# Kernel tuning notes

Measured on AMD Instinct MI355X. Metric: run time of the kernel, lower is better.

Reference implementation:

```python
import jax, jax.numpy as jnp
import numpy as np

D = 512      # dim_model
F = 2048     # dim_feedforward
E = 8        # num_experts
K = 2        # num_experts_per_token
B, S = 2, 4096


def setup_inputs() -> dict:
    key = jax.random.key(0)
    ks = jax.random.split(key, 8)
    sd = 1.0 / np.sqrt(D)
    sf = 1.0 / np.sqrt(F)
    return {
        "x": jax.random.normal(ks[0], (B, S, D), dtype=jnp.float32),
        "router_w": jax.random.uniform(ks[1], (D, E), jnp.float32, -sd, sd),
        "router_b": jax.random.uniform(ks[2], (E,), jnp.float32, -sd, sd),
        "w1": jax.random.uniform(ks[3], (E, D, F), jnp.float32, -sd, sd),
        "b1": jax.random.uniform(ks[4], (E, F), jnp.float32, -sd, sd),
        "w2": jax.random.uniform(ks[5], (E, F, D), jnp.float32, -sf, sf),
        "b2": jax.random.uniform(ks[6], (E, D), jnp.float32, -sf, sf),
    }


def reference(x, router_w, router_b, w1, b1, w2, b2):
    orig_shape = x.shape
    flat = x.reshape(-1, orig_shape[-1])                     # [T, D]
    logits = flat @ router_w + router_b                      # [T, E]
    gates = jax.nn.softmax(logits, axis=-1)                  # [T, E]
    top_vals, top_idx = jax.lax.top_k(gates, K)              # [T, K]
    top_vals = top_vals / jnp.sum(top_vals, axis=-1, keepdims=True)
    # combine weight per (token, expert): zero for unselected experts,
    # so dense per-expert evaluation yields identical math to masked dispatch.
    onehot = jax.nn.one_hot(top_idx, E, dtype=flat.dtype)    # [T, K, E]
    comb = jnp.einsum('tk,tke->te', top_vals, onehot)        # [T, E]
    # expert FFNs over all tokens (dropout is identity in eval)
    hidden = jax.nn.relu(jnp.einsum('td,edf->etf', flat, w1) + b1[:, None, :])  # [E, T, F]
    eout = jnp.einsum('etf,efd->etd', hidden, w2) + b2[:, None, :]              # [E, T, D]
    out = jnp.einsum('te,etd->td', comb, eout)               # [T, D]
    return out.reshape(orig_shape)
```

## Files before the change

kernel.cpp:

```cpp
#include <hip/hip_runtime.h>
#include <cstdint>
#include <cstddef>

#define TD 512
#define TF 2048
#define NE 8
#define NT 8192
#define CAP 17408

using u16 = unsigned short;
using u32 = unsigned int;

typedef __attribute__((ext_vector_type(8))) __bf16 bf16x8;
typedef __attribute__((ext_vector_type(4))) float f32x4;

__device__ __forceinline__ u16 f2bf(float f) {
  u32 u = __float_as_uint(f);
  u32 r = (u + 0x7fffu + ((u >> 16) & 1u)) >> 16;
  return (u16)r;
}

__device__ __forceinline__ void load_lds16(const void* g, void* l) {
  __builtin_amdgcn_global_load_lds(
      (const __attribute__((address_space(1))) void*)g,
      (__attribute__((address_space(3))) void*)l, 16, 0, 0);
}

__global__ void zero_kernel(float* __restrict__ out) {
  int i = blockIdx.x * 256 + threadIdx.x;
  float4 z = make_float4(0.f, 0.f, 0.f, 0.f);
  *reinterpret_cast<float4*>(out + (size_t)i * 4) = z;
}

__global__ void transpose_cvt_kernel(const float* __restrict__ in, u16* __restrict__ out,
                                     int R, int C) {
  __shared__ u16 tile[32][33];
  int c0 = blockIdx.x * 32, r0 = blockIdx.y * 32;
  const float* ib = in + (size_t)blockIdx.z * R * C;
  u16* ob = out + (size_t)blockIdx.z * R * C;
  #pragma unroll
  for (int rr = 0; rr < 32; rr += 8) {
    int r = r0 + threadIdx.y + rr;
    int c = c0 + threadIdx.x;
    tile[threadIdx.y + rr][threadIdx.x] = f2bf(ib[(size_t)r * C + c]);
  }
  __syncthreads();
  #pragma unroll
  for (int rr = 0; rr < 32; rr += 8) {
    int oc = c0 + threadIdx.y + rr;
    int orr = r0 + threadIdx.x;
    ob[(size_t)oc * R + orr] = tile[threadIdx.x][threadIdx.y + rr];
  }
}

__global__ void router_kernel(const float* __restrict__ x, const float* __restrict__ rw,
                              const float* __restrict__ rb, int2* __restrict__ tokE,
                              float2* __restrict__ tokG, u16* __restrict__ xb) {
  int wv = threadIdx.x >> 6;
  int lane = threadIdx.x & 63;
  int t = blockIdx.x * 4 + wv;
  const float* xr = x + (size_t)t * TD;
  float4 a0 = *reinterpret_cast<const float4*>(xr + lane * 4);
  float4 a1 = *reinterpret_cast<const float4*>(xr + 256 + lane * 4);
  {
    u16 o[8];
    o[0] = f2bf(a0.x); o[1] = f2bf(a0.y); o[2] = f2bf(a0.z); o[3] = f2bf(a0.w);
    o[4] = f2bf(a1.x); o[5] = f2bf(a1.y); o[6] = f2bf(a1.z); o[7] = f2bf(a1.w);
    u16* xo = xb + (size_t)t * TD;
    *reinterpret_cast<uint2*>(xo + lane * 4) = *reinterpret_cast<uint2*>(o);
    *reinterpret_cast<uint2*>(xo + 256 + lane * 4) = *reinterpret_cast<uint2*>(o + 4);
  }
  float p[NE];
  #pragma unroll
  for (int e = 0; e < NE; e++) p[e] = 0.f;
  float av[8] = {a0.x, a0.y, a0.z, a0.w, a1.x, a1.y, a1.z, a1.w};
  #pragma unroll
  for (int j = 0; j < 8; j++) {
    int d = (j < 4) ? (lane * 4 + j) : (256 + lane * 4 + j - 4);
    const float* r = rw + (size_t)d * NE;
    #pragma unroll
    for (int e = 0; e < NE; e++) p[e] += av[j] * r[e];
  }
  #pragma unroll
  for (int off = 32; off >= 1; off >>= 1) {
    #pragma unroll
    for (int e = 0; e < NE; e++) p[e] += __shfl_xor(p[e], off);
  }
  if (lane == 0) {
    float l[NE];
    #pragma unroll
    for (int e = 0; e < NE; e++) l[e] = p[e] + rb[e];
    float m = l[0];
    #pragma unroll
    for (int e = 1; e < NE; e++) m = fmaxf(m, l[e]);
    float g[NE];
    #pragma unroll
    for (int e = 0; e < NE; e++) g[e] = __expf(l[e] - m);
    int i0 = 0;
    #pragma unroll
    for (int e = 1; e < NE; e++) if (g[e] > g[i0]) i0 = e;
    int i1 = -1;
    #pragma unroll
    for (int e = 0; e < NE; e++) {
      if (e == i0) continue;
      if (i1 < 0 || g[e] > g[i1]) i1 = e;
    }
    float inv = 1.f / (g[i0] + g[i1]);
    tokE[t] = make_int2(i0, i1);
    tokG[t] = make_float2(g[i0] * inv, g[i1] * inv);
  }
}

__global__ void count_offsets_kernel(const int2* __restrict__ tokE, int* __restrict__ offs,
                                     int* __restrict__ cursors) {
  __shared__ int hist[NE];
  if (threadIdx.x < NE) {
    hist[threadIdx.x] = 0;
    cursors[threadIdx.x * 16] = 0;
  }
  __syncthreads();
  for (int t = threadIdx.x; t < NT; t += 1024) {
    int2 e = tokE[t];
    atomicAdd(&hist[e.x], 1);
    atomicAdd(&hist[e.y], 1);
  }
  __syncthreads();
  if (threadIdx.x == 0) {
    int tot = 0;
    for (int e = 0; e < NE; e++) {
      offs[e] = tot;
      tot += (hist[e] + 127) & ~127;
    }
    offs[NE] = tot;
  }
}

__global__ void fill_kernel(const int* __restrict__ offs, int* __restrict__ tok,
                            float* __restrict__ gate, int* __restrict__ sexp) {
  int s = blockIdx.x * 256 + threadIdx.x;
  int e = NE - 1;
  #pragma unroll
  for (int i = 0; i < NE; i++)
    if (s >= offs[i] && s < offs[i + 1]) e = i;
  sexp[s] = e;
  tok[s] = -1;
  gate[s] = 0.f;
}

__global__ void scatter_kernel(const int2* __restrict__ tokE, const float2* __restrict__ tokG,
                               const int* __restrict__ offs, int* __restrict__ cursors,
                               int* __restrict__ tok, float* __restrict__ gate) {
  int t = blockIdx.x * 256 + threadIdx.x;
  int lane = threadIdx.x & 63;
  int2 e = tokE[t];
  float2 g = tokG[t];
  #pragma unroll
  for (int k = 0; k < 2; k++) {
    int ek = k ? e.y : e.x;
    float gk = k ? g.y : g.x;
    #pragma unroll
    for (int ex = 0; ex < NE; ex++) {
      unsigned long long mask = __ballot(ek == ex);
      if (ek == ex) {
        int leader = __ffsll(mask) - 1;
        int rank = __popcll(mask & ((1ull << lane) - 1ull));
        int base = 0;
        if (lane == leader) base = atomicAdd(&cursors[ex * 16], __popcll(mask));
        base = __shfl(base, leader);
        int s = offs[ex] + base + rank;
        tok[s] = t;
        gate[s] = gk;
      }
    }
  }
}

__global__ __launch_bounds__(256, 4) void gemm1_kernel(
    const u16* __restrict__ xb, const u16* __restrict__ w1t,
    const float* __restrict__ b1, const int* __restrict__ tok,
    const int* __restrict__ sexp, u16* __restrict__ H) {
  __shared__ u16 As[128 * 64];
  __shared__ u16 Bs[128 * 64];
  __shared__ int tokS[128];
  const int tid = threadIdx.x;
  const int s0 = blockIdx.x * 128;
  const int f0 = blockIdx.y * 128;
  const int e = sexp[s0];
  if (tid < 128) {
    int t = tok[s0 + tid];
    tokS[tid] = t < 0 ? 0 : t;
  }
  __syncthreads();

  const int lane = tid & 63;
  const int wv = tid >> 6;
  const int srow = lane >> 3;
  const int scol = (((lane & 7) ^ srow) & 7) * 8;
  const int wm = (wv >> 1) * 64;
  const int wn = (wv & 1) * 64;
  const int mrow = lane & 15;
  const int quad = lane >> 4;
  const int rq = mrow & 7;

  f32x4 zero = {0.f, 0.f, 0.f, 0.f};
  f32x4 acc[4][4];
  #pragma unroll
  for (int i = 0; i < 4; i++)
    #pragma unroll
    for (int j = 0; j < 4; j++) acc[i][j] = zero;

  const u16* bbase = w1t + ((size_t)e * TF + f0) * TD;

  for (int k0 = 0; k0 < TD; k0 += 64) {
    if (k0) __syncthreads();
    #pragma unroll
    for (int p = 0; p < 4; p++) {
      int row = wv * 32 + p * 8 + srow;
      load_lds16(xb + (size_t)tokS[row] * TD + k0 + scol, &As[(wv * 32 + p * 8) * 64]);
      load_lds16(bbase + (size_t)row * TD + k0 + scol, &Bs[(wv * 32 + p * 8) * 64]);
    }
    __syncthreads();
    #pragma unroll
    for (int ks = 0; ks < 2; ks++) {
      bf16x8 a[4], b[4];
      #pragma unroll
      for (int i = 0; i < 4; i++)
        a[i] = *reinterpret_cast<const bf16x8*>(
            &As[(wm + i * 16 + mrow) * 64 + ((ks * 4 + quad) ^ rq) * 8]);
      #pragma unroll
      for (int j = 0; j < 4; j++)
        b[j] = *reinterpret_cast<const bf16x8*>(
            &Bs[(wn + j * 16 + mrow) * 64 + ((ks * 4 + quad) ^ rq) * 8]);
      #pragma unroll
      for (int i = 0; i < 4; i++)
        #pragma unroll
        for (int j = 0; j < 4; j++)
          acc[i][j] = __builtin_amdgcn_mfma_f32_16x16x32_bf16(a[i], b[j], acc[i][j], 0, 0, 0);
    }
  }

  float bv[4];
  #pragma unroll
  for (int j = 0; j < 4; j++) bv[j] = b1[e * TF + f0 + wn + j * 16 + mrow];
  #pragma unroll
  for (int i = 0; i < 4; i++) {
    #pragma unroll
    for (int r = 0; r < 4; r++) {
      int row = s0 + wm + i * 16 + quad * 4 + r;
      u16* hrow = H + (size_t)row * TF + f0;
      #pragma unroll
      for (int j = 0; j < 4; j++) {
        float v = acc[i][j][r] + bv[j];
        v = v > 0.f ? v : 0.f;
        hrow[wn + j * 16 + mrow] = f2bf(v);
      }
    }
  }
}

__global__ __launch_bounds__(256, 4) void gemm2_kernel(
    const u16* __restrict__ H, const u16* __restrict__ w2t,
    const float* __restrict__ b2, const int* __restrict__ tok,
    const float* __restrict__ gate, const int* __restrict__ sexp,
    float* __restrict__ out) {
  __shared__ u16 As[128 * 64];
  __shared__ u16 Bs[128 * 64];
  __shared__ int tokS[128];
  __shared__ float gateS[128];
  const int tid = threadIdx.x;
  const int s0 = blockIdx.x * 128;
  const int d0 = blockIdx.y * 128;
  const int kz = blockIdx.z;
  const int e = sexp[s0];
  if (tid < 128) {
    tokS[tid] = tok[s0 + tid];
    gateS[tid] = gate[s0 + tid];
  }
  __syncthreads();

  const int lane = tid & 63;
  const int wv = tid >> 6;
  const int srow = lane >> 3;
  const int scol = (((lane & 7) ^ srow) & 7) * 8;
  const int wm = (wv >> 1) * 64;
  const int wn = (wv & 1) * 64;
  const int mrow = lane & 15;
  const int quad = lane >> 4;
  const int rq = mrow & 7;

  f32x4 zero = {0.f, 0.f, 0.f, 0.f};
  f32x4 acc[4][4];
  #pragma unroll
  for (int i = 0; i < 4; i++)
    #pragma unroll
    for (int j = 0; j < 4; j++) acc[i][j] = zero;

  const u16* bbase = w2t + ((size_t)e * TD + d0) * TF;
  const int kbeg = kz * (TF / 2);
  const int kend = kbeg + (TF / 2);

  for (int k0 = kbeg; k0 < kend; k0 += 64) {
    if (k0 != kbeg) __syncthreads();
    #pragma unroll
    for (int p = 0; p < 4; p++) {
      int row = wv * 32 + p * 8 + srow;
      load_lds16(H + (size_t)(s0 + row) * TF + k0 + scol, &As[(wv * 32 + p * 8) * 64]);
      load_lds16(bbase + (size_t)row * TF + k0 + scol, &Bs[(wv * 32 + p * 8) * 64]);
    }
    __syncthreads();
    #pragma unroll
    for (int ks = 0; ks < 2; ks++) {
      bf16x8 a[4], b[4];
      #pragma unroll
      for (int i = 0; i < 4; i++)
        a[i] = *reinterpret_cast<const bf16x8*>(
            &As[(wm + i * 16 + mrow) * 64 + ((ks * 4 + quad) ^ rq) * 8]);
      #pragma unroll
      for (int j = 0; j < 4; j++)
        b[j] = *reinterpret_cast<const bf16x8*>(
            &Bs[(wn + j * 16 + mrow) * 64 + ((ks * 4 + quad) ^ rq) * 8]);
      #pragma unroll
      for (int i = 0; i < 4; i++)
        #pragma unroll
        for (int j = 0; j < 4; j++)
          acc[i][j] = __builtin_amdgcn_mfma_f32_16x16x32_bf16(a[i], b[j], acc[i][j], 0, 0, 0);
    }
  }

  float bv[4];
  #pragma unroll
  for (int j = 0; j < 4; j++)
    bv[j] = (kz == 0) ? b2[e * TD + d0 + wn + j * 16 + mrow] : 0.f;
  #pragma unroll
  for (int i = 0; i < 4; i++) {
    #pragma unroll
    for (int r = 0; r < 4; r++) {
      int rl = wm + i * 16 + quad * 4 + r;
      int t = tokS[rl];
      if (t < 0) continue;
      float g = gateS[rl];
      float* orow = out + (size_t)t * TD + d0;
      #pragma unroll
      for (int j = 0; j < 4; j++) {
        atomicAdd(&orow[wn + j * 16 + mrow], g * (acc[i][j][r] + bv[j]));
      }
    }
  }
}

extern "C" void kernel_launch(void* const* d_in, const int* in_sizes, int n_in,
                              void* d_out, int out_size, void* d_ws, size_t ws_size,
                              hipStream_t stream) {
  const float* x  = (const float*)d_in[0];
  const float* rw = (const float*)d_in[1];
  const float* rb = (const float*)d_in[2];
  const float* w1 = (const float*)d_in[3];
  const float* b1 = (const float*)d_in[4];
  const float* w2 = (const float*)d_in[5];
  const float* b2 = (const float*)d_in[6];
  float* out = (float*)d_out;

  char* w = (char*)d_ws;
  u16* xb   = (u16*)w;            w += (size_t)NT * TD * 2;
  u16* w1t  = (u16*)w;            w += (size_t)NE * TD * TF * 2;
  u16* w2t  = (u16*)w;            w += (size_t)NE * TF * TD * 2;
  u16* H    = (u16*)w;            w += (size_t)CAP * TF * 2;
  int* tok  = (int*)w;            w += (size_t)CAP * 4;
  float* gate = (float*)w;        w += (size_t)CAP * 4;
  int* sexp = (int*)w;            w += (size_t)CAP * 4;
  int2* tokE = (int2*)w;          w += (size_t)NT * 8;
  float2* tokG = (float2*)w;      w += (size_t)NT * 8;
  int* cursors = (int*)w;         w += 1024;
  int* offs = (int*)w;            w += 256;

  zero_kernel<<<dim3((NT * TD) / (256 * 4)), dim3(256), 0, stream>>>(out);
  transpose_cvt_kernel<<<dim3(TF / 32, TD / 32, NE), dim3(32, 8), 0, stream>>>(w1, w1t, TD, TF);
  transpose_cvt_kernel<<<dim3(TD / 32, TF / 32, NE), dim3(32, 8), 0, stream>>>(w2, w2t, TF, TD);
  router_kernel<<<dim3(NT / 4), dim3(256), 0, stream>>>(x, rw, rb, tokE, tokG, xb);
  count_offsets_kernel<<<dim3(1), dim3(1024), 0, stream>>>(tokE, offs, cursors);
  fill_kernel<<<dim3(CAP / 256), dim3(256), 0, stream>>>(offs, tok, gate, sexp);
  scatter_kernel<<<dim3(NT / 256), dim3(256), 0, stream>>>(tokE, tokG, offs, cursors, tok, gate);
  gemm1_kernel<<<dim3(CAP / 128, TF / 128), dim3(256), 0, stream>>>(xb, w1t, b1, tok, sexp, H);
  gemm2_kernel<<<dim3(CAP / 128, TD / 128, 2), dim3(256), 0, stream>>>(H, w2t, b2, tok, gate, sexp, out);
}
```

Before: 326.2 us.

## Replace atomic scatter-add in expert GEMM2 with bf16 expert output and gather combine

GEMM2 no longer uses split-K or atomically accumulates gated results into the output. It writes each slot's expert output as bf16 into a new buffer, and a new combine kernel gathers each token's two slots through a slot-index map and applies the gates. This drops the zero-fill kernel, the float atomics and the split-K duplication. The cost is an extra bf16 round trip through memory, one more kernel launch, and GEMM2 now launching half as many blocks. Launch bounds are also lowered from 4 to 3 blocks per CU.

```diff
diff --git a/kernel.cpp b/kernel.cpp
--- a/kernel.cpp
+++ b/kernel.cpp
@@ -20,16 +20,14 @@
   return (u16)r;
 }
 
+__device__ __forceinline__ float bf2f(u16 b) {
+  return __uint_as_float((u32)b << 16);
+}
+
 __device__ __forceinline__ void load_lds16(const void* g, void* l) {
   __builtin_amdgcn_global_load_lds(
       (const __attribute__((address_space(1))) void*)g,
       (__attribute__((address_space(3))) void*)l, 16, 0, 0);
-}
-
-__global__ void zero_kernel(float* __restrict__ out) {
-  int i = blockIdx.x * 256 + threadIdx.x;
-  float4 z = make_float4(0.f, 0.f, 0.f, 0.f);
-  *reinterpret_cast<float4*>(out + (size_t)i * 4) = z;
 }
 
 __global__ void transpose_cvt_kernel(const float* __restrict__ in, u16* __restrict__ out,
@@ -136,7 +134,7 @@
 }
 
 __global__ void fill_kernel(const int* __restrict__ offs, int* __restrict__ tok,
-                            float* __restrict__ gate, int* __restrict__ sexp) {
+                            int* __restrict__ sexp) {
   int s = blockIdx.x * 256 + threadIdx.x;
   int e = NE - 1;
   #pragma unroll
@@ -144,20 +142,17 @@
     if (s >= offs[i] && s < offs[i + 1]) e = i;
   sexp[s] = e;
   tok[s] = -1;
-  gate[s] = 0.f;
-}
-
-__global__ void scatter_kernel(const int2* __restrict__ tokE, const float2* __restrict__ tokG,
+}
+
+__global__ void scatter_kernel(const int2* __restrict__ tokE,
                                const int* __restrict__ offs, int* __restrict__ cursors,
-                               int* __restrict__ tok, float* __restrict__ gate) {
+                               int* __restrict__ tok, int* __restrict__ slotOf) {
   int t = blockIdx.x * 256 + threadIdx.x;
   int lane = threadIdx.x & 63;
   int2 e = tokE[t];
-  float2 g = tokG[t];
   #pragma unroll
   for (int k = 0; k < 2; k++) {
     int ek = k ? e.y : e.x;
-    float gk = k ? g.y : g.x;
     #pragma unroll
     for (int ex = 0; ex < NE; ex++) {
       unsigned long long mask = __ballot(ek == ex);
@@ -169,13 +164,13 @@
         base = __shfl(base, leader);
         int s = offs[ex] + base + rank;
         tok[s] = t;
-        gate[s] = gk;
+        slotOf[t * 2 + k] = s;
       }
     }
   }
 }
 
-__global__ __launch_bounds__(256, 4) void gemm1_kernel(
+__global__ __launch_bounds__(256, 3) void gemm1_kernel(
     const u16* __restrict__ xb, const u16* __restrict__ w1t,
     const float* __restrict__ b1, const int* __restrict__ tok,
     const int* __restrict__ sexp, u16* __restrict__ H) {
@@ -258,25 +253,16 @@
   }
 }
 
-__global__ __launch_bounds__(256, 4) void gemm2_kernel(
+__global__ __launch_bounds__(256, 3) void gemm2_kernel(
     const u16* __restrict__ H, const u16* __restrict__ w2t,
-    const float* __restrict__ b2, const int* __restrict__ tok,
-    const float* __restrict__ gate, const int* __restrict__ sexp,
-    float* __restrict__ out) {
+    const float* __restrict__ b2, const int* __restrict__ sexp,
+    u16* __restrict__ eout) {
   __shared__ u16 As[128 * 64];
   __shared__ u16 Bs[128 * 64];
-  __shared__ int tokS[128];
-  __shared__ float gateS[128];
   const int tid = threadIdx.x;
   const int s0 = blockIdx.x * 128;
   const int d0 = blockIdx.y * 128;
-  const int kz = blockIdx.z;
   const int e = sexp[s0];
-  if (tid < 128) {
-    tokS[tid] = tok[s0 + tid];
-    gateS[tid] = gate[s0 + tid];
-  }
-  __syncthreads();
 
   const int lane = tid & 63;
   const int wv = tid >> 6;
@@ -296,11 +282,9 @@
     for (int j = 0; j < 4; j++) acc[i][j] = zero;
 
   const u16* bbase = w2t + ((size_t)e * TD + d0) * TF;
-  const int kbeg = kz * (TF / 2);
-  const int kend = kbeg + (TF / 2);
-
-  for (int k0 = kbeg; k0 < kend; k0 += 64) {
-    if (k0 != kbeg) __syncthreads();
+
+  for (int k0 = 0; k0 < TF; k0 += 64) {
+    if (k0) __syncthreads();
     #pragma unroll
     for (int p = 0; p < 4; p++) {
       int row = wv * 32 + p * 8 + srow;
@@ -329,23 +313,39 @@
 
   float bv[4];
   #pragma unroll
-  for (int j = 0; j < 4; j++)
-    bv[j] = (kz == 0) ? b2[e * TD + d0 + wn + j * 16 + mrow] : 0.f;
+  for (int j = 0; j < 4; j++) bv[j] = b2[e * TD + d0 + wn + j * 16 + mrow];
   #pragma unroll
   for (int i = 0; i < 4; i++) {
     #pragma unroll
     for (int r = 0; r < 4; r++) {
-      int rl = wm + i * 16 + quad * 4 + r;
-      int t = tokS[rl];
-      if (t < 0) continue;
-      float g = gateS[rl];
-      float* orow = out + (size_t)t * TD + d0;
+      int row = s0 + wm + i * 16 + quad * 4 + r;
+      u16* orow = eout + (size_t)row * TD + d0;
       #pragma unroll
       for (int j = 0; j < 4; j++) {
-        atomicAdd(&orow[wn + j * 16 + mrow], g * (acc[i][j][r] + bv[j]));
+        orow[wn + j * 16 + mrow] = f2bf(acc[i][j][r] + bv[j]);
       }
     }
   }
+}
+
+__global__ void combine_kernel(const u16* __restrict__ eout, const int* __restrict__ slotOf,
+                               const float2* __restrict__ tokG, float* __restrict__ out) {
+  int wv = threadIdx.x >> 6;
+  int lane = threadIdx.x & 63;
+  int t = blockIdx.x * 4 + wv;
+  int sA = slotOf[t * 2];
+  int sB = slotOf[t * 2 + 1];
+  float2 g = tokG[t];
+  uint4 ua = *reinterpret_cast<const uint4*>(eout + (size_t)sA * TD + lane * 8);
+  uint4 ub = *reinterpret_cast<const uint4*>(eout + (size_t)sB * TD + lane * 8);
+  const u16* pa = reinterpret_cast<const u16*>(&ua);
+  const u16* pb = reinterpret_cast<const u16*>(&ub);
+  float o[8];
+  #pragma unroll
+  for (int k = 0; k < 8; k++) o[k] = g.x * bf2f(pa[k]) + g.y * bf2f(pb[k]);
+  float* od = out + (size_t)t * TD + lane * 8;
+  *reinterpret_cast<float4*>(od) = make_float4(o[0], o[1], o[2], o[3]);
+  *reinterpret_cast<float4*>(od + 4) = make_float4(o[4], o[5], o[6], o[7]);
 }
 
 extern "C" void kernel_launch(void* const* d_in, const int* in_sizes, int n_in,
@@ -365,21 +365,22 @@
   u16* w1t  = (u16*)w;            w += (size_t)NE * TD * TF * 2;
   u16* w2t  = (u16*)w;            w += (size_t)NE * TF * TD * 2;
   u16* H    = (u16*)w;            w += (size_t)CAP * TF * 2;
+  u16* eout = (u16*)w;            w += (size_t)CAP * TD * 2;
   int* tok  = (int*)w;            w += (size_t)CAP * 4;
-  float* gate = (float*)w;        w += (size_t)CAP * 4;
   int* sexp = (int*)w;            w += (size_t)CAP * 4;
+  int* slotOf = (int*)w;          w += (size_t)NT * 2 * 4;
   int2* tokE = (int2*)w;          w += (size_t)NT * 8;
   float2* tokG = (float2*)w;      w += (size_t)NT * 8;
   int* cursors = (int*)w;         w += 1024;
   int* offs = (int*)w;            w += 256;
 
-  zero_kernel<<<dim3((NT * TD) / (256 * 4)), dim3(256), 0, stream>>>(out);
   transpose_cvt_kernel<<<dim3(TF / 32, TD / 32, NE), dim3(32, 8), 0, stream>>>(w1, w1t, TD, TF);
   transpose_cvt_kernel<<<dim3(TD / 32, TF / 32, NE), dim3(32, 8), 0, stream>>>(w2, w2t, TF, TD);
   router_kernel<<<dim3(NT / 4), dim3(256), 0, stream>>>(x, rw, rb, tokE, tokG, xb);
   count_offsets_kernel<<<dim3(1), dim3(1024), 0, stream>>>(tokE, offs, cursors);
-  fill_kernel<<<dim3(CAP / 256), dim3(256), 0, stream>>>(offs, tok, gate, sexp);
-  scatter_kernel<<<dim3(NT / 256), dim3(256), 0, stream>>>(tokE, tokG, offs, cursors, tok, gate);
+  fill_kernel<<<dim3(CAP / 256), dim3(256), 0, stream>>>(offs, tok, sexp);
+  scatter_kernel<<<dim3(NT / 256), dim3(256), 0, stream>>>(tokE, offs, cursors, tok, slotOf);
   gemm1_kernel<<<dim3(CAP / 128, TF / 128), dim3(256), 0, stream>>>(xb, w1t, b1, tok, sexp, H);
-  gemm2_kernel<<<dim3(CAP / 128, TD / 128, 2), dim3(256), 0, stream>>>(H, w2t, b2, tok, gate, sexp, out);
-}
+  gemm2_kernel<<<dim3(CAP / 128, TD / 128), dim3(256), 0, stream>>>(H, w2t, b2, sexp, eout);
+  combine_kernel<<<dim3(NT / 4), dim3(256), 0, stream>>>(eout, slotOf, tokG, out);
+}
```

After: 268.8 us. 17.6% less time.
